# Kernel tuning notes

Hardware: AMD Instinct MI355X
Metric: run time of the kernel (lower is better)

Reference implementation:

```python
import jax, jax.numpy as jnp
import numpy as np

N_NODES = 100000
N_EDGES = 1600000
N_GRAPHS = 128
IN_F, H_F, OUT_F, HID, NCLS = 128, 128, 64, 10, 10

def setup_inputs() -> dict:
    key = jax.random.key(0)
    ks = jax.random.split(key, 12)
    feats = jax.random.normal(ks[0], (N_NODES, IN_F), dtype=jnp.float32)
    src = jax.random.randint(ks[1], (N_EDGES,), 0, N_NODES, dtype=jnp.int32)
    dst = jax.random.randint(ks[2], (N_EDGES,), 0, N_NODES, dtype=jnp.int32)
    graph_ids = jnp.sort(jax.random.randint(ks[3], (N_NODES,), 0, N_GRAPHS, dtype=jnp.int32))
    def glorot(k, shape):
        fan = shape[0] + shape[1]
        return jax.random.normal(k, shape, dtype=jnp.float32) * jnp.sqrt(2.0 / fan)
    return {
        'feats': feats, 'src': src, 'dst': dst, 'graph_ids': graph_ids,
        'W1': glorot(ks[4], (IN_F, H_F)), 'b1': jnp.zeros((H_F,), jnp.float32),
        'W2': glorot(ks[5], (H_F, OUT_F)), 'b2': jnp.zeros((OUT_F,), jnp.float32),
        'fcW1': glorot(ks[6], (OUT_F, HID)), 'fcb1': jnp.zeros((HID,), jnp.float32),
        'fcW2': glorot(ks[7], (HID, NCLS)), 'fcb2': jnp.zeros((NCLS,), jnp.float32),
    }

def _graph_conv(x, W, b, src, dst):
    # DGL GraphConv, norm='both': D_dst^{-1/2} A D_src^{-1/2} X W + b
    ones = jnp.ones((src.shape[0],), x.dtype)
    deg_out = jnp.clip(jax.ops.segment_sum(ones, src, num_segments=N_NODES), 1.0)
    deg_in = jnp.clip(jax.ops.segment_sum(ones, dst, num_segments=N_NODES), 1.0)
    x = x * jax.lax.rsqrt(deg_out)[:, None]
    m = jax.ops.segment_sum(x[src], dst, num_segments=N_NODES)  # gather-scatter over edges
    m = m * jax.lax.rsqrt(deg_in)[:, None]
    return m @ W + b

def reference(feats, src, dst, graph_ids, W1, b1, W2, b2, fcW1, fcb1, fcW2, fcb2):
    h = jax.nn.relu(_graph_conv(feats, W1, b1, src, dst))
    h = jax.nn.relu(_graph_conv(h, W2, b2, src, dst))
    # dgl.mean_nodes: per-graph mean pooling
    sums = jax.ops.segment_sum(h, graph_ids, num_segments=N_GRAPHS)
    counts = jnp.clip(jax.ops.segment_sum(jnp.ones((N_NODES,), h.dtype), graph_ids, num_segments=N_GRAPHS), 1.0)
    pooled = sums / counts[:, None]  # [G, OUT_F]
    z = jax.nn.relu(pooled @ fcW1 + fcb1)
    return jax.nn.softmax(z @ fcW2 + fcb2, axis=1)
```

## Files before the change

kernel.cpp:

```cpp
#include <hip/hip_runtime.h>
#include <hip/hip_bf16.h>

#define N_NODES 100000
#define N_EDGES 1600000
#define N_GRAPHS 128
#define IN_F 128
#define H_F 128
#define OUT_F 64
#define HID 10
#define NCLS 10
#define XPAD 136
#define BSH 7
#define NBUCK 782
#define SBLK 128
#define EPB (N_EDGES / SBLK)
#define NB_PREP 4
#define PCHUNK 8

typedef __attribute__((ext_vector_type(8))) short bf16x8;
typedef __attribute__((ext_vector_type(4))) float f32x4;
typedef __attribute__((ext_vector_type(2))) float f32x2;

__device__ __forceinline__ float bl(unsigned int u) { return __uint_as_float(u << 16); }
__device__ __forceinline__ float bh(unsigned int u) { return __uint_as_float(u & 0xffff0000u); }

__global__ __launch_bounds__(1024) void k_hist2(const int* __restrict__ src, const int* __restrict__ dst,
                                                int* __restrict__ Pd, int* __restrict__ Ps,
                                                const float* __restrict__ W1, const float* __restrict__ W2,
                                                unsigned short* __restrict__ Wt1, unsigned short* __restrict__ Wt2) {
    __shared__ int hd[NBUCK];
    __shared__ int hs[NBUCK];
    const int blk = blockIdx.x;
    if (blk < SBLK) {
        for (int i = threadIdx.x; i < NBUCK; i += 1024) { hd[i] = 0; hs[i] = 0; }
        __syncthreads();
        const int base = blk * EPB;
        for (int i = threadIdx.x; i < EPB; i += 1024) {
            atomicAdd(&hd[dst[base + i] >> BSH], 1);
            atomicAdd(&hs[src[base + i] >> BSH], 1);
        }
        __syncthreads();
        for (int b = threadIdx.x; b < NBUCK; b += 1024) {
            Pd[b * SBLK + blk] = hd[b];
            Ps[b * SBLK + blk] = hs[b];
        }
    } else {
        int t = (blk - SBLK) * 1024 + threadIdx.x;
        const int stride = NB_PREP * 1024;
        for (int i = t; i < 128 * 128; i += stride) {
            int c = i >> 7, k = i & 127;
            __hip_bfloat16 v = __float2bfloat16(W1[k * 128 + c]);
            Wt1[i] = *(unsigned short*)&v;
        }
        for (int i = t; i < 64 * 128; i += stride) {
            int c = i >> 7, k = i & 127;
            __hip_bfloat16 v = __float2bfloat16(W2[k * 64 + c]);
            Wt2[i] = *(unsigned short*)&v;
        }
    }
}

__global__ __launch_bounds__(128) void k_scanA(int* __restrict__ Pd, int* __restrict__ Ps,
                                               int* __restrict__ Td, int* __restrict__ Ts) {
    __shared__ int sc[128];
    const int b = blockIdx.x;
    const int t = threadIdx.x;
    int* P = (b < NBUCK) ? Pd : Ps;
    int* T = (b < NBUCK) ? Td : Ts;
    const int bb = (b < NBUCK) ? b : b - NBUCK;
    int v = P[bb * SBLK + t];
    sc[t] = v;
    __syncthreads();
    for (int off = 1; off < 128; off <<= 1) {
        int u = (t >= off) ? sc[t - off] : 0;
        __syncthreads();
        sc[t] += u;
        __syncthreads();
    }
    P[bb * SBLK + t] = sc[t] - v;
    if (t == 127) T[bb] = sc[127];
}

__global__ __launch_bounds__(1024) void k_scanB(const int* __restrict__ Td, const int* __restrict__ Ts,
                                                int* __restrict__ Bd, int* __restrict__ Bs) {
    __shared__ int sc[1024];
    const int t = threadIdx.x;
    int v = (t < NBUCK) ? Td[t] : 0;
    sc[t] = v;
    __syncthreads();
    for (int off = 1; off < 1024; off <<= 1) {
        int u = (t >= off) ? sc[t - off] : 0;
        __syncthreads();
        sc[t] += u;
        __syncthreads();
    }
    if (t < NBUCK) Bd[t] = sc[t] - v;
    if (t == NBUCK - 1) Bd[NBUCK] = sc[t];
    __syncthreads();
    int v2 = (t < NBUCK) ? Ts[t] : 0;
    sc[t] = v2;
    __syncthreads();
    for (int off = 1; off < 1024; off <<= 1) {
        int u = (t >= off) ? sc[t - off] : 0;
        __syncthreads();
        sc[t] += u;
        __syncthreads();
    }
    if (t < NBUCK) Bs[t] = sc[t] - v2;
    if (t == NBUCK - 1) Bs[NBUCK] = sc[t];
}

__global__ __launch_bounds__(1024) void k_scatter(const int* __restrict__ src, const int* __restrict__ dst,
                                                  const int* __restrict__ Pd, const int* __restrict__ Ps,
                                                  const int* __restrict__ Bd, const int* __restrict__ Bs,
                                                  unsigned int* __restrict__ pb, unsigned char* __restrict__ sb) {
    __shared__ int tk[NBUCK];
    const int b = blockIdx.x;
    const bool isPb = b < SBLK;
    const int blk = isPb ? b : b - SBLK;
    for (int i = threadIdx.x; i < NBUCK; i += 1024) tk[i] = 0;
    __syncthreads();
    const int base = blk * EPB;
    if (isPb) {
        for (int i = threadIdx.x; i < EPB; i += 1024) {
            int d = dst[base + i];
            int s = src[base + i];
            int bd = d >> BSH;
            int t = atomicAdd(&tk[bd], 1);
            pb[Bd[bd] + Pd[bd * SBLK + blk] + t] = ((unsigned)s << 7) | (unsigned)(d & 127);
        }
    } else {
        for (int i = threadIdx.x; i < EPB; i += 1024) {
            int s = src[base + i];
            int bs = s >> BSH;
            int t = atomicAdd(&tk[bs], 1);
            sb[Bs[bs] + Ps[bs * SBLK + blk] + t] = (unsigned char)(s & 127);
        }
    }
}

__global__ __launch_bounds__(256) void k_finalize(const unsigned int* __restrict__ pb, const int* __restrict__ Bd,
                                                  const unsigned char* __restrict__ sb, const int* __restrict__ Bs,
                                                  int* __restrict__ rp, int* __restrict__ cnt_out,
                                                  int* __restrict__ cols) {
    __shared__ int cnt[128];
    __shared__ int exc[128];
    __shared__ int tick[128];
    __shared__ int h[128];
    __shared__ int sc[128];
    const int b = blockIdx.x;
    const int tid = threadIdx.x;
    if (tid < 128) { cnt[tid] = 0; tick[tid] = 0; h[tid] = 0; }
    __syncthreads();
    const int e0 = Bd[b], e1 = Bd[b + 1];
    for (int i = e0 + tid; i < e1; i += 256) atomicAdd(&cnt[pb[i] & 127], 1);
    const int f0 = Bs[b], f1 = Bs[b + 1];
    for (int i = f0 + tid; i < f1; i += 256) atomicAdd(&h[sb[i]], 1);
    __syncthreads();
    if (tid < 128) sc[tid] = cnt[tid];
    __syncthreads();
    for (int off = 1; off < 128; off <<= 1) {
        int u = (tid < 128 && tid >= off) ? sc[tid - off] : 0;
        __syncthreads();
        if (tid < 128) sc[tid] += u;
        __syncthreads();
    }
    if (tid < 128) exc[tid] = sc[tid] - cnt[tid];
    __syncthreads();
    const int node0 = b << BSH;
    if (tid < 128 && node0 + tid < N_NODES) {
        rp[node0 + tid] = e0 + exc[tid];
        cnt_out[node0 + tid] = h[tid];
    }
    if (b == NBUCK - 1 && tid == 0) rp[N_NODES] = N_EDGES;
    for (int i = e0 + tid; i < e1; i += 256) {
        unsigned int p = pb[i];
        int loc = p & 127;
        int t = atomicAdd(&tick[loc], 1);
        cols[e0 + exc[loc] + t] = (int)(p >> 7);
    }
}

__global__ __launch_bounds__(256) void k_gemm1(const float* __restrict__ X,
                                               const unsigned short* __restrict__ Wt,
                                               const int* __restrict__ cnt_out,
                                               unsigned char* __restrict__ Gout) {
    __shared__ __align__(16) unsigned short Xs[32 * XPAD];
    __shared__ __align__(16) unsigned short Ws[128 * XPAD];
    const int tid = threadIdx.x;
    const int row0 = blockIdx.x * 32;

    {
        const float4* X4 = (const float4*)X;
#pragma unroll
        for (int j = 0; j < 4; j++) {
            int i = tid + 256 * j;
            int r = i >> 5, k4 = i & 31;
            float4 x = X4[(size_t)(row0 + r) * 32 + k4];
            __hip_bfloat162 lo = __float22bfloat162_rn({x.x, x.y});
            __hip_bfloat162 hi = __float22bfloat162_rn({x.z, x.w});
            uint2 u;
            u.x = *(unsigned int*)&lo;
            u.y = *(unsigned int*)&hi;
            *(uint2*)&Xs[r * XPAD + k4 * 4] = u;
        }
    }
    {
        const uint2* W2 = (const uint2*)Wt;
#pragma unroll
        for (int j = 0; j < 16; j++) {
            int i = tid + 256 * j;
            int cc = i >> 5, kk = i & 31;
            uint2 u = W2[(size_t)cc * 32 + kk];
            *(uint2*)&Ws[cc * XPAD + kk * 4] = u;
        }
    }
    __syncthreads();

    const int lane = tid & 63;
    const int wv = tid >> 6;
    const int m = lane & 15;
    const int q = lane >> 4;
    const int cg = wv * 32;

    f32x4 acc00 = {0.f, 0.f, 0.f, 0.f}, acc01 = {0.f, 0.f, 0.f, 0.f};
    f32x4 acc10 = {0.f, 0.f, 0.f, 0.f}, acc11 = {0.f, 0.f, 0.f, 0.f};
#pragma unroll
    for (int ks = 0; ks < 4; ks++) {
        int kb = ks * 32 + q * 8;
        bf16x8 a0 = *(const bf16x8*)&Xs[m * XPAD + kb];
        bf16x8 a1 = *(const bf16x8*)&Xs[(16 + m) * XPAD + kb];
        bf16x8 b0 = *(const bf16x8*)&Ws[(cg + m) * XPAD + kb];
        bf16x8 b1 = *(const bf16x8*)&Ws[(cg + 16 + m) * XPAD + kb];
        acc00 = __builtin_amdgcn_mfma_f32_16x16x32_bf16(a0, b0, acc00, 0, 0, 0);
        acc01 = __builtin_amdgcn_mfma_f32_16x16x32_bf16(a0, b1, acc01, 0, 0, 0);
        acc10 = __builtin_amdgcn_mfma_f32_16x16x32_bf16(a1, b0, acc10, 0, 0, 0);
        acc11 = __builtin_amdgcn_mfma_f32_16x16x32_bf16(a1, b1, acc11, 0, 0, 0);
    }
#pragma unroll
    for (int r = 0; r < 4; r++) {
        int rowA = row0 + q * 4 + r;
        int rowB = rowA + 16;
        float sA = rsqrtf((float)max(cnt_out[rowA], 1));
        float sB = rsqrtf((float)max(cnt_out[rowB], 1));
        unsigned int pkA = __builtin_amdgcn_cvt_pk_fp8_f32(acc00[r] * sA, acc01[r] * sA, 0, false);
        unsigned int pkB = __builtin_amdgcn_cvt_pk_fp8_f32(acc10[r] * sB, acc11[r] * sB, 0, false);
        unsigned char* gA = Gout + (size_t)rowA * 128 + cg + m;
        gA[0]  = (unsigned char)(pkA & 0xffu);
        gA[16] = (unsigned char)((pkA >> 8) & 0xffu);
        unsigned char* gB = Gout + (size_t)rowB * 128 + cg + m;
        gB[0]  = (unsigned char)(pkB & 0xffu);
        gB[16] = (unsigned char)((pkB >> 8) & 0xffu);
    }
}

template <int TOTF, bool XBF16, bool OUT_FP8>
__global__ __launch_bounds__(256) void k_gemm_mfma(const void* __restrict__ Xv,
                                                   const unsigned short* __restrict__ Wt,
                                                   const int* __restrict__ cnt_out,
                                                   void* __restrict__ GoutV) {
    __shared__ __align__(16) unsigned short Xs[32 * XPAD];
    __shared__ __align__(16) unsigned short Ws[64 * XPAD];
    const int tid = threadIdx.x;
    const int cbase = blockIdx.y * 64;
    const int row0 = blockIdx.x * 32;

    if constexpr (XBF16) {
        const uint2* X2 = (const uint2*)Xv;
#pragma unroll
        for (int j = 0; j < 4; j++) {
            int i = tid + 256 * j;
            int r = i >> 5, kk = i & 31;
            uint2 u = X2[(size_t)(row0 + r) * 32 + kk];
            *(uint2*)&Xs[r * XPAD + kk * 4] = u;
        }
    } else {
        const float4* X4 = (const float4*)Xv;
#pragma unroll
        for (int j = 0; j < 4; j++) {
            int i = tid + 256 * j;
            int r = i >> 5, k4 = i & 31;
            float4 x = X4[(size_t)(row0 + r) * 32 + k4];
            __hip_bfloat162 lo = __float22bfloat162_rn({x.x, x.y});
            __hip_bfloat162 hi = __float22bfloat162_rn({x.z, x.w});
            uint2 u;
            u.x = *(unsigned int*)&lo;
            u.y = *(unsigned int*)&hi;
            *(uint2*)&Xs[r * XPAD + k4 * 4] = u;
        }
    }
    {
        const uint2* W2 = (const uint2*)Wt;
#pragma unroll
        for (int j = 0; j < 8; j++) {
            int i = tid + 256 * j;
            int c = i >> 5, kk = i & 31;
            uint2 u = W2[(size_t)(cbase + c) * 32 + kk];
            *(uint2*)&Ws[c * XPAD + kk * 4] = u;
        }
    }
    __syncthreads();

    const int lane = tid & 63;
    const int wv = tid >> 6;
    const int m = lane & 15;
    const int q = lane >> 4;
    const int roff = (wv & 1) * 16;
    const int coff = (wv >> 1) * 32;

    f32x4 acc0 = {0.f, 0.f, 0.f, 0.f}, acc1 = {0.f, 0.f, 0.f, 0.f};
#pragma unroll
    for (int ks = 0; ks < 4; ks++) {
        int kb = ks * 32 + q * 8;
        bf16x8 a  = *(const bf16x8*)&Xs[(roff + m) * XPAD + kb];
        bf16x8 b0 = *(const bf16x8*)&Ws[(coff + m) * XPAD + kb];
        bf16x8 b1 = *(const bf16x8*)&Ws[(coff + 16 + m) * XPAD + kb];
        acc0 = __builtin_amdgcn_mfma_f32_16x16x32_bf16(a, b0, acc0, 0, 0, 0);
        acc1 = __builtin_amdgcn_mfma_f32_16x16x32_bf16(a, b1, acc1, 0, 0, 0);
    }
#pragma unroll
    for (int r = 0; r < 4; r++) {
        int row = row0 + roff + q * 4 + r;
        float s = rsqrtf((float)max(cnt_out[row], 1));
        int col0 = cbase + coff + m;
        if constexpr (OUT_FP8) {
            unsigned int pk = __builtin_amdgcn_cvt_pk_fp8_f32(acc0[r] * s, acc1[r] * s, 0, false);
            unsigned char* gp = (unsigned char*)GoutV + (size_t)row * TOTF + col0;
            gp[0]  = (unsigned char)(pk & 0xffu);
            gp[16] = (unsigned char)((pk >> 8) & 0xffu);
        } else {
            unsigned short* Gout = (unsigned short*)GoutV;
            __hip_bfloat16 o0 = __float2bfloat16(acc0[r] * s);
            __hip_bfloat16 o1 = __float2bfloat16(acc1[r] * s);
            Gout[(size_t)row * TOTF + col0]      = *(unsigned short*)&o0;
            Gout[(size_t)row * TOTF + col0 + 16] = *(unsigned short*)&o1;
        }
    }
}

__global__ __launch_bounds__(256) void k_spmm128f8(const unsigned short* __restrict__ G,
                                                   const int* __restrict__ rp,
                                                   const int* __restrict__ cols,
                                                   const float* __restrict__ bias,
                                                   unsigned int* __restrict__ H) {
    const int lane = threadIdx.x & 63;
    const int wave = threadIdx.x >> 6;
    const int v = blockIdx.x * 4 + wave;
    const int b0 = __builtin_amdgcn_readfirstlane(rp[v]);
    const int e0 = __builtin_amdgcn_readfirstlane(rp[v + 1]);
    const int deg = e0 - b0;
    const unsigned short* gl = G + lane;
    f32x2 acc = {0.f, 0.f};
    int j = 0;
    while (j + 16 <= deg) {
        unsigned int u[16];
#pragma unroll
        for (int k = 0; k < 16; k++) {
            int s = cols[b0 + j + k];
            u[k] = gl[(size_t)s * 64];
        }
#pragma unroll
        for (int k = 0; k < 16; k++) acc += __builtin_amdgcn_cvt_pk_f32_fp8(u[k], false);
        j += 16;
    }
    if (j + 8 <= deg) {
        unsigned int u[8];
#pragma unroll
        for (int k = 0; k < 8; k++) { int s = cols[b0 + j + k]; u[k] = gl[(size_t)s * 64]; }
#pragma unroll
        for (int k = 0; k < 8; k++) acc += __builtin_amdgcn_cvt_pk_f32_fp8(u[k], false);
        j += 8;
    }
    if (j + 4 <= deg) {
        unsigned int u[4];
#pragma unroll
        for (int k = 0; k < 4; k++) { int s = cols[b0 + j + k]; u[k] = gl[(size_t)s * 64]; }
#pragma unroll
        for (int k = 0; k < 4; k++) acc += __builtin_amdgcn_cvt_pk_f32_fp8(u[k], false);
        j += 4;
    }
    if (j + 2 <= deg) {
        unsigned int u0, u1;
        { int s = cols[b0 + j];     u0 = gl[(size_t)s * 64]; }
        { int s = cols[b0 + j + 1]; u1 = gl[(size_t)s * 64]; }
        acc += __builtin_amdgcn_cvt_pk_f32_fp8(u0, false);
        acc += __builtin_amdgcn_cvt_pk_f32_fp8(u1, false);
        j += 2;
    }
    if (j < deg) {
        int s = cols[b0 + j];
        unsigned int u = gl[(size_t)s * 64];
        acc += __builtin_amdgcn_cvt_pk_f32_fp8(u, false);
    }
    const float rs = rsqrtf((float)max(deg, 1));
    const float2 bb = *(const float2*)&bias[2 * lane];
    __hip_bfloat162 p = __float22bfloat162_rn({fmaxf(fmaf(acc.x, rs, bb.x), 0.f),
                                               fmaxf(fmaf(acc.y, rs, bb.y), 0.f)});
    H[(size_t)v * 64 + lane] = *(unsigned int*)&p;
}

__global__ __launch_bounds__(256) void k_spmm64f8(const unsigned char* __restrict__ G,
                                                  const int* __restrict__ rp,
                                                  const int* __restrict__ cols,
                                                  const float* __restrict__ bias,
                                                  unsigned short* __restrict__ H) {
    const int lane = threadIdx.x & 63;
    const int wave = threadIdx.x >> 6;
    const int v = blockIdx.x * 4 + wave;
    const int b0 = __builtin_amdgcn_readfirstlane(rp[v]);
    const int e0 = __builtin_amdgcn_readfirstlane(rp[v + 1]);
    const int deg = e0 - b0;
    const unsigned char* gl = G + lane;
    f32x2 acc = {0.f, 0.f};
    int j = 0;
    while (j + 16 <= deg) {
        unsigned int u[16];
#pragma unroll
        for (int k = 0; k < 16; k++) {
            int s = cols[b0 + j + k];
            u[k] = gl[(size_t)s * 64];
        }
#pragma unroll
        for (int k = 0; k < 16; k++) acc += __builtin_amdgcn_cvt_pk_f32_fp8(u[k], false);
        j += 16;
    }
    if (j + 8 <= deg) {
        unsigned int u[8];
#pragma unroll
        for (int k = 0; k < 8; k++) { int s = cols[b0 + j + k]; u[k] = gl[(size_t)s * 64]; }
#pragma unroll
        for (int k = 0; k < 8; k++) acc += __builtin_amdgcn_cvt_pk_f32_fp8(u[k], false);
        j += 8;
    }
    if (j + 4 <= deg) {
        unsigned int u[4];
#pragma unroll
        for (int k = 0; k < 4; k++) { int s = cols[b0 + j + k]; u[k] = gl[(size_t)s * 64]; }
#pragma unroll
        for (int k = 0; k < 4; k++) acc += __builtin_amdgcn_cvt_pk_f32_fp8(u[k], false);
        j += 4;
    }
    if (j + 2 <= deg) {
        unsigned int u0, u1;
        { int s = cols[b0 + j];     u0 = gl[(size_t)s * 64]; }
        { int s = cols[b0 + j + 1]; u1 = gl[(size_t)s * 64]; }
        acc += __builtin_amdgcn_cvt_pk_f32_fp8(u0, false);
        acc += __builtin_amdgcn_cvt_pk_f32_fp8(u1, false);
        j += 2;
    }
    if (j < deg) {
        int s = cols[b0 + j];
        unsigned int u = gl[(size_t)s * 64];
        acc += __builtin_amdgcn_cvt_pk_f32_fp8(u, false);
    }
    const float rs = rsqrtf((float)max(deg, 1));
    const float b = bias[lane];
    __hip_bfloat16 o = __float2bfloat16(fmaxf(fmaf(acc.x, rs, b), 0.f));
    H[(size_t)v * 64 + lane] = *(unsigned short*)&o;
}

__global__ __launch_bounds__(256) void k_pool(const unsigned short* __restrict__ h2,
                                              const int* __restrict__ gid,
                                              float* __restrict__ part) {
    __shared__ int se[2];
    __shared__ float red[16][16][4];
    const int cpart = blockIdx.x;
    const int g = blockIdx.y;
    const int tid = threadIdx.x;
    if (tid < 2) {
        int target = g + tid;
        int lo = 0, hi = N_NODES;
        while (lo < hi) {
            int mid = (lo + hi) >> 1;
            if (gid[mid] < target) lo = mid + 1; else hi = mid;
        }
        se[tid] = lo;
    }
    __syncthreads();
    const int s = se[0], e = se[1];
    const int chunk = (e - s + PCHUNK - 1) / PCHUNK;
    const int lo = s + cpart * chunk;
    const int hi = min(lo + chunk, e);
    const int r = tid >> 4, cp = tid & 15;
    float a0 = 0.f, a1 = 0.f, a2 = 0.f, a3 = 0.f;
    const uint2* H = (const uint2*)h2;
    for (int v = lo + r; v < hi; v += 16) {
        uint2 u = H[(size_t)v * 16 + cp];
        a0 += bl(u.x); a1 += bh(u.x); a2 += bl(u.y); a3 += bh(u.y);
    }
    red[r][cp][0] = a0; red[r][cp][1] = a1; red[r][cp][2] = a2; red[r][cp][3] = a3;
    for (int off = 8; off > 0; off >>= 1) {
        __syncthreads();
        if (r < off) {
#pragma unroll
            for (int k = 0; k < 4; k++) red[r][cp][k] += red[r + off][cp][k];
        }
    }
    __syncthreads();
    if (r == 0) {
        float4 o = {red[0][cp][0], red[0][cp][1], red[0][cp][2], red[0][cp][3]};
        *(float4*)&part[((size_t)cpart * N_GRAPHS + g) * 64 + 4 * cp] = o;
    }
}

__global__ __launch_bounds__(64) void k_mlp(const float* __restrict__ part,
                                            const int* __restrict__ gid,
                                            const float* __restrict__ fcW1,
                                            const float* __restrict__ fcb1,
                                            const float* __restrict__ fcW2,
                                            const float* __restrict__ fcb2,
                                            float* __restrict__ out) {
    __shared__ int se[2];
    __shared__ float p[64];
    __shared__ float z[10];
    __shared__ float l[10];
    __shared__ float red[2];
    const int g = blockIdx.x;
    const int t = threadIdx.x;
    if (t < 2) {
        int target = g + t;
        int lo = 0, hi = N_NODES;
        while (lo < hi) {
            int mid = (lo + hi) >> 1;
            if (gid[mid] < target) lo = mid + 1; else hi = mid;
        }
        se[t] = lo;
    }
    __syncthreads();
    const int cnt = max(se[1] - se[0], 1);
    float a = 0.f;
#pragma unroll
    for (int c = 0; c < PCHUNK; c++) a += part[((size_t)c * N_GRAPHS + g) * 64 + t];
    p[t] = a / (float)cnt;
    __syncthreads();
    if (t < 10) {
        float acc = fcb1[t];
        for (int k = 0; k < 64; k++) acc = fmaf(p[k], fcW1[k * 10 + t], acc);
        z[t] = fmaxf(acc, 0.f);
    }
    __syncthreads();
    if (t < 10) {
        float acc = fcb2[t];
        for (int k = 0; k < 10; k++) acc = fmaf(z[k], fcW2[k * 10 + t], acc);
        l[t] = acc;
    }
    __syncthreads();
    if (t == 0) {
        float m = l[0];
        for (int i = 1; i < 10; i++) m = fmaxf(m, l[i]);
        float ssum = 0.f;
        for (int i = 0; i < 10; i++) ssum += expf(l[i] - m);
        red[0] = m;
        red[1] = ssum;
    }
    __syncthreads();
    if (t < 10) out[g * 10 + t] = expf(l[t] - red[0]) / red[1];
}

extern "C" void kernel_launch(void* const* d_in, const int* in_sizes, int n_in,
                              void* d_out, int out_size, void* d_ws, size_t ws_size,
                              hipStream_t stream) {
    const float* feats = (const float*)d_in[0];
    const int* src = (const int*)d_in[1];
    const int* dst = (const int*)d_in[2];
    const int* gid = (const int*)d_in[3];
    const float* W1 = (const float*)d_in[4];
    const float* b1 = (const float*)d_in[5];
    const float* W2 = (const float*)d_in[6];
    const float* b2 = (const float*)d_in[7];
    const float* fcW1 = (const float*)d_in[8];
    const float* fcb1 = (const float*)d_in[9];
    const float* fcW2 = (const float*)d_in[10];
    const float* fcb2 = (const float*)d_in[11];
    float* out = (float*)d_out;

    char* w = (char*)d_ws;
    size_t off = 0;
    auto alloc = [&](size_t bytes) -> void* {
        void* p = w + off;
        off = (off + bytes + 255) & ~(size_t)255;
        return p;
    };
    int* cnt_out = (int*)alloc(N_NODES * 4);
    int* rp      = (int*)alloc((N_NODES + 1) * 4);
    int* cols    = (int*)alloc((size_t)N_EDGES * 4);
    int* Pd      = (int*)alloc(NBUCK * SBLK * 4);
    int* Ps      = (int*)alloc(NBUCK * SBLK * 4);
    int* Td      = (int*)alloc(NBUCK * 4);
    int* Ts      = (int*)alloc(NBUCK * 4);
    int* Bd      = (int*)alloc((NBUCK + 1) * 4);
    int* Bs      = (int*)alloc((NBUCK + 1) * 4);
    unsigned int* pb  = (unsigned int*)alloc((size_t)N_EDGES * 4);
    unsigned char* sb = (unsigned char*)alloc((size_t)N_EDGES);
    unsigned short* Wt1 = (unsigned short*)alloc(128 * 128 * 2);
    unsigned short* Wt2 = (unsigned short*)alloc(64 * 128 * 2);
    unsigned char* g1 = (unsigned char*)alloc((size_t)N_NODES * 128);
    unsigned short* h1 = (unsigned short*)alloc((size_t)N_NODES * 128 * 2);
    unsigned char* g2 = (unsigned char*)alloc((size_t)N_NODES * 64);
    unsigned short* h2 = (unsigned short*)alloc((size_t)N_NODES * 64 * 2);
    float* part = (float*)alloc((size_t)PCHUNK * N_GRAPHS * 64 * 4);

    k_hist2<<<SBLK + NB_PREP, 1024, 0, stream>>>(src, dst, Pd, Ps, W1, W2, Wt1, Wt2);
    k_scanA<<<2 * NBUCK, 128, 0, stream>>>(Pd, Ps, Td, Ts);
    k_scanB<<<1, 1024, 0, stream>>>(Td, Ts, Bd, Bs);
    k_scatter<<<2 * SBLK, 1024, 0, stream>>>(src, dst, Pd, Ps, Bd, Bs, pb, sb);
    k_finalize<<<NBUCK, 256, 0, stream>>>(pb, Bd, sb, Bs, rp, cnt_out, cols);

    k_gemm1<<<N_NODES / 32, 256, 0, stream>>>(feats, Wt1, cnt_out, g1);
    k_spmm128f8<<<N_NODES / 4, 256, 0, stream>>>((const unsigned short*)g1, rp, cols, b1, (unsigned int*)h1);

    k_gemm_mfma<64, true, true><<<dim3(N_NODES / 32, 1), 256, 0, stream>>>(h1, Wt2, cnt_out, g2);
    k_spmm64f8<<<N_NODES / 4, 256, 0, stream>>>(g2, rp, cols, b2, (unsigned short*)h2);

    k_pool<<<dim3(PCHUNK, N_GRAPHS), 256, 0, stream>>>(h2, gid, part);
    k_mlp<<<N_GRAPHS, 64, 0, stream>>>(part, gid, fcW1, fcb1, fcW2, fcb2, out);
}
```

Baseline: 279.7 us.

## Compute out-degree with global atomics and process two nodes per wave in SpMM

Out-degree counting moves from a bucketed sort pass (src histogram, scan, byte scatter, per-bucket count) to direct global atomic increments into a zeroed count array, which removes half of the CSR-build work. Both SpMM kernels now have each wave handle two consecutive destination nodes, interleaving their gathers in blocks of eight, to raise memory-level parallelism and halve the block count. The trade-offs are global atomic contention on 100k counters and a larger per-wave register footprint, plus extra tail code.

```diff
diff --git a/kernel.cpp b/kernel.cpp
--- a/kernel.cpp
+++ b/kernel.cpp
@@ -24,26 +24,28 @@
 __device__ __forceinline__ float bl(unsigned int u) { return __uint_as_float(u << 16); }
 __device__ __forceinline__ float bh(unsigned int u) { return __uint_as_float(u & 0xffff0000u); }
 
+__global__ __launch_bounds__(256) void k_zero(int* __restrict__ p, int n) {
+    int i = blockIdx.x * 256 + threadIdx.x;
+    int stride = gridDim.x * 256;
+    for (; i < n; i += stride) p[i] = 0;
+}
+
 __global__ __launch_bounds__(1024) void k_hist2(const int* __restrict__ src, const int* __restrict__ dst,
-                                                int* __restrict__ Pd, int* __restrict__ Ps,
+                                                int* __restrict__ Pd, int* __restrict__ cnt_out,
                                                 const float* __restrict__ W1, const float* __restrict__ W2,
                                                 unsigned short* __restrict__ Wt1, unsigned short* __restrict__ Wt2) {
     __shared__ int hd[NBUCK];
-    __shared__ int hs[NBUCK];
     const int blk = blockIdx.x;
     if (blk < SBLK) {
-        for (int i = threadIdx.x; i < NBUCK; i += 1024) { hd[i] = 0; hs[i] = 0; }
+        for (int i = threadIdx.x; i < NBUCK; i += 1024) hd[i] = 0;
         __syncthreads();
         const int base = blk * EPB;
         for (int i = threadIdx.x; i < EPB; i += 1024) {
             atomicAdd(&hd[dst[base + i] >> BSH], 1);
-            atomicAdd(&hs[src[base + i] >> BSH], 1);
-        }
-        __syncthreads();
-        for (int b = threadIdx.x; b < NBUCK; b += 1024) {
-            Pd[b * SBLK + blk] = hd[b];
-            Ps[b * SBLK + blk] = hs[b];
-        }
+            atomicAdd(&cnt_out[src[base + i]], 1);
+        }
+        __syncthreads();
+        for (int b = threadIdx.x; b < NBUCK; b += 1024) Pd[b * SBLK + blk] = hd[b];
     } else {
         int t = (blk - SBLK) * 1024 + threadIdx.x;
         const int stride = NB_PREP * 1024;
@@ -60,15 +62,11 @@
     }
 }
 
-__global__ __launch_bounds__(128) void k_scanA(int* __restrict__ Pd, int* __restrict__ Ps,
-                                               int* __restrict__ Td, int* __restrict__ Ts) {
+__global__ __launch_bounds__(128) void k_scanA(int* __restrict__ Pd, int* __restrict__ Td) {
     __shared__ int sc[128];
     const int b = blockIdx.x;
     const int t = threadIdx.x;
-    int* P = (b < NBUCK) ? Pd : Ps;
-    int* T = (b < NBUCK) ? Td : Ts;
-    const int bb = (b < NBUCK) ? b : b - NBUCK;
-    int v = P[bb * SBLK + t];
+    int v = Pd[b * SBLK + t];
     sc[t] = v;
     __syncthreads();
     for (int off = 1; off < 128; off <<= 1) {
@@ -77,12 +75,11 @@
         sc[t] += u;
         __syncthreads();
     }
-    P[bb * SBLK + t] = sc[t] - v;
-    if (t == 127) T[bb] = sc[127];
-}
-
-__global__ __launch_bounds__(1024) void k_scanB(const int* __restrict__ Td, const int* __restrict__ Ts,
-                                                int* __restrict__ Bd, int* __restrict__ Bs) {
+    Pd[b * SBLK + t] = sc[t] - v;
+    if (t == 127) Td[b] = sc[127];
+}
+
+__global__ __launch_bounds__(1024) void k_scanB(const int* __restrict__ Td, int* __restrict__ Bd) {
     __shared__ int sc[1024];
     const int t = threadIdx.x;
     int v = (t < NBUCK) ? Td[t] : 0;
@@ -96,66 +93,37 @@
     }
     if (t < NBUCK) Bd[t] = sc[t] - v;
     if (t == NBUCK - 1) Bd[NBUCK] = sc[t];
-    __syncthreads();
-    int v2 = (t < NBUCK) ? Ts[t] : 0;
-    sc[t] = v2;
-    __syncthreads();
-    for (int off = 1; off < 1024; off <<= 1) {
-        int u = (t >= off) ? sc[t - off] : 0;
-        __syncthreads();
-        sc[t] += u;
-        __syncthreads();
-    }
-    if (t < NBUCK) Bs[t] = sc[t] - v2;
-    if (t == NBUCK - 1) Bs[NBUCK] = sc[t];
 }
 
 __global__ __launch_bounds__(1024) void k_scatter(const int* __restrict__ src, const int* __restrict__ dst,
-                                                  const int* __restrict__ Pd, const int* __restrict__ Ps,
-                                                  const int* __restrict__ Bd, const int* __restrict__ Bs,
-                                                  unsigned int* __restrict__ pb, unsigned char* __restrict__ sb) {
+                                                  const int* __restrict__ Pd, const int* __restrict__ Bd,
+                                                  unsigned int* __restrict__ pb) {
     __shared__ int tk[NBUCK];
-    const int b = blockIdx.x;
-    const bool isPb = b < SBLK;
-    const int blk = isPb ? b : b - SBLK;
+    const int blk = blockIdx.x;
     for (int i = threadIdx.x; i < NBUCK; i += 1024) tk[i] = 0;
     __syncthreads();
     const int base = blk * EPB;
-    if (isPb) {
-        for (int i = threadIdx.x; i < EPB; i += 1024) {
-            int d = dst[base + i];
-            int s = src[base + i];
-            int bd = d >> BSH;
-            int t = atomicAdd(&tk[bd], 1);
-            pb[Bd[bd] + Pd[bd * SBLK + blk] + t] = ((unsigned)s << 7) | (unsigned)(d & 127);
-        }
-    } else {
-        for (int i = threadIdx.x; i < EPB; i += 1024) {
-            int s = src[base + i];
-            int bs = s >> BSH;
-            int t = atomicAdd(&tk[bs], 1);
-            sb[Bs[bs] + Ps[bs * SBLK + blk] + t] = (unsigned char)(s & 127);
-        }
+    for (int i = threadIdx.x; i < EPB; i += 1024) {
+        int d = dst[base + i];
+        int s = src[base + i];
+        int bd = d >> BSH;
+        int t = atomicAdd(&tk[bd], 1);
+        pb[Bd[bd] + Pd[bd * SBLK + blk] + t] = ((unsigned)s << 7) | (unsigned)(d & 127);
     }
 }
 
 __global__ __launch_bounds__(256) void k_finalize(const unsigned int* __restrict__ pb, const int* __restrict__ Bd,
-                                                  const unsigned char* __restrict__ sb, const int* __restrict__ Bs,
-                                                  int* __restrict__ rp, int* __restrict__ cnt_out,
-                                                  int* __restrict__ cols) {
+                                                  int* __restrict__ rp, int* __restrict__ cols) {
     __shared__ int cnt[128];
     __shared__ int exc[128];
     __shared__ int tick[128];
-    __shared__ int h[128];
     __shared__ int sc[128];
     const int b = blockIdx.x;
     const int tid = threadIdx.x;
-    if (tid < 128) { cnt[tid] = 0; tick[tid] = 0; h[tid] = 0; }
+    if (tid < 128) { cnt[tid] = 0; tick[tid] = 0; }
     __syncthreads();
     const int e0 = Bd[b], e1 = Bd[b + 1];
     for (int i = e0 + tid; i < e1; i += 256) atomicAdd(&cnt[pb[i] & 127], 1);
-    const int f0 = Bs[b], f1 = Bs[b + 1];
-    for (int i = f0 + tid; i < f1; i += 256) atomicAdd(&h[sb[i]], 1);
     __syncthreads();
     if (tid < 128) sc[tid] = cnt[tid];
     __syncthreads();
@@ -168,10 +136,7 @@
     if (tid < 128) exc[tid] = sc[tid] - cnt[tid];
     __syncthreads();
     const int node0 = b << BSH;
-    if (tid < 128 && node0 + tid < N_NODES) {
-        rp[node0 + tid] = e0 + exc[tid];
-        cnt_out[node0 + tid] = h[tid];
-    }
+    if (tid < 128 && node0 + tid < N_NODES) rp[node0 + tid] = e0 + exc[tid];
     if (b == NBUCK - 1 && tid == 0) rp[N_NODES] = N_EDGES;
     for (int i = e0 + tid; i < e1; i += 256) {
         unsigned int p = pb[i];
@@ -338,6 +303,88 @@
     }
 }
 
+__device__ __forceinline__ void tail128(const unsigned short* __restrict__ gl, const int* __restrict__ cols,
+                                        int b, int d, int j, f32x2& acc) {
+    while (j + 16 <= d) {
+        unsigned int u[16];
+#pragma unroll
+        for (int k = 0; k < 16; k++) { int s = cols[b + j + k]; u[k] = gl[(size_t)s * 64]; }
+#pragma unroll
+        for (int k = 0; k < 16; k++) acc += __builtin_amdgcn_cvt_pk_f32_fp8(u[k], false);
+        j += 16;
+    }
+    if (j + 8 <= d) {
+        unsigned int u[8];
+#pragma unroll
+        for (int k = 0; k < 8; k++) { int s = cols[b + j + k]; u[k] = gl[(size_t)s * 64]; }
+#pragma unroll
+        for (int k = 0; k < 8; k++) acc += __builtin_amdgcn_cvt_pk_f32_fp8(u[k], false);
+        j += 8;
+    }
+    if (j + 4 <= d) {
+        unsigned int u[4];
+#pragma unroll
+        for (int k = 0; k < 4; k++) { int s = cols[b + j + k]; u[k] = gl[(size_t)s * 64]; }
+#pragma unroll
+        for (int k = 0; k < 4; k++) acc += __builtin_amdgcn_cvt_pk_f32_fp8(u[k], false);
+        j += 4;
+    }
+    if (j + 2 <= d) {
+        unsigned int u0, u1;
+        { int s = cols[b + j];     u0 = gl[(size_t)s * 64]; }
+        { int s = cols[b + j + 1]; u1 = gl[(size_t)s * 64]; }
+        acc += __builtin_amdgcn_cvt_pk_f32_fp8(u0, false);
+        acc += __builtin_amdgcn_cvt_pk_f32_fp8(u1, false);
+        j += 2;
+    }
+    if (j < d) {
+        int s = cols[b + j];
+        unsigned int u = gl[(size_t)s * 64];
+        acc += __builtin_amdgcn_cvt_pk_f32_fp8(u, false);
+    }
+}
+
+__device__ __forceinline__ void tail64(const unsigned char* __restrict__ gl, const int* __restrict__ cols,
+                                       int b, int d, int j, f32x2& acc) {
+    while (j + 16 <= d) {
+        unsigned int u[16];
+#pragma unroll
+        for (int k = 0; k < 16; k++) { int s = cols[b + j + k]; u[k] = gl[(size_t)s * 64]; }
+#pragma unroll
+        for (int k = 0; k < 16; k++) acc += __builtin_amdgcn_cvt_pk_f32_fp8(u[k], false);
+        j += 16;
+    }
+    if (j + 8 <= d) {
+        unsigned int u[8];
+#pragma unroll
+        for (int k = 0; k < 8; k++) { int s = cols[b + j + k]; u[k] = gl[(size_t)s * 64]; }
+#pragma unroll
+        for (int k = 0; k < 8; k++) acc += __builtin_amdgcn_cvt_pk_f32_fp8(u[k], false);
+        j += 8;
+    }
+    if (j + 4 <= d) {
+        unsigned int u[4];
+#pragma unroll
+        for (int k = 0; k < 4; k++) { int s = cols[b + j + k]; u[k] = gl[(size_t)s * 64]; }
+#pragma unroll
+        for (int k = 0; k < 4; k++) acc += __builtin_amdgcn_cvt_pk_f32_fp8(u[k], false);
+        j += 4;
+    }
+    if (j + 2 <= d) {
+        unsigned int u0, u1;
+        { int s = cols[b + j];     u0 = gl[(size_t)s * 64]; }
+        { int s = cols[b + j + 1]; u1 = gl[(size_t)s * 64]; }
+        acc += __builtin_amdgcn_cvt_pk_f32_fp8(u0, false);
+        acc += __builtin_amdgcn_cvt_pk_f32_fp8(u1, false);
+        j += 2;
+    }
+    if (j < d) {
+        int s = cols[b + j];
+        unsigned int u = gl[(size_t)s * 64];
+        acc += __builtin_amdgcn_cvt_pk_f32_fp8(u, false);
+    }
+}
+
 __global__ __launch_bounds__(256) void k_spmm128f8(const unsigned short* __restrict__ G,
                                                    const int* __restrict__ rp,
                                                    const int* __restrict__ cols,
@@ -345,58 +392,43 @@
                                                    unsigned int* __restrict__ H) {
     const int lane = threadIdx.x & 63;
     const int wave = threadIdx.x >> 6;
-    const int v = blockIdx.x * 4 + wave;
-    const int b0 = __builtin_amdgcn_readfirstlane(rp[v]);
-    const int e0 = __builtin_amdgcn_readfirstlane(rp[v + 1]);
-    const int deg = e0 - b0;
+    const int v0 = (blockIdx.x * 4 + wave) * 2;
+    const int b0 = __builtin_amdgcn_readfirstlane(rp[v0]);
+    const int b1 = __builtin_amdgcn_readfirstlane(rp[v0 + 1]);
+    const int e1 = __builtin_amdgcn_readfirstlane(rp[v0 + 2]);
+    const int dA = b1 - b0, dB = e1 - b1;
     const unsigned short* gl = G + lane;
-    f32x2 acc = {0.f, 0.f};
-    int j = 0;
-    while (j + 16 <= deg) {
-        unsigned int u[16];
-#pragma unroll
-        for (int k = 0; k < 16; k++) {
-            int s = cols[b0 + j + k];
-            u[k] = gl[(size_t)s * 64];
-        }
-#pragma unroll
-        for (int k = 0; k < 16; k++) acc += __builtin_amdgcn_cvt_pk_f32_fp8(u[k], false);
-        j += 16;
-    }
-    if (j + 8 <= deg) {
-        unsigned int u[8];
-#pragma unroll
-        for (int k = 0; k < 8; k++) { int s = cols[b0 + j + k]; u[k] = gl[(size_t)s * 64]; }
-#pragma unroll
-        for (int k = 0; k < 8; k++) acc += __builtin_amdgcn_cvt_pk_f32_fp8(u[k], false);
-        j += 8;
-    }
-    if (j + 4 <= deg) {
-        unsigned int u[4];
-#pragma unroll
-        for (int k = 0; k < 4; k++) { int s = cols[b0 + j + k]; u[k] = gl[(size_t)s * 64]; }
-#pragma unroll
-        for (int k = 0; k < 4; k++) acc += __builtin_amdgcn_cvt_pk_f32_fp8(u[k], false);
-        j += 4;
-    }
-    if (j + 2 <= deg) {
-        unsigned int u0, u1;
-        { int s = cols[b0 + j];     u0 = gl[(size_t)s * 64]; }
-        { int s = cols[b0 + j + 1]; u1 = gl[(size_t)s * 64]; }
-        acc += __builtin_amdgcn_cvt_pk_f32_fp8(u0, false);
-        acc += __builtin_amdgcn_cvt_pk_f32_fp8(u1, false);
-        j += 2;
-    }
-    if (j < deg) {
-        int s = cols[b0 + j];
-        unsigned int u = gl[(size_t)s * 64];
-        acc += __builtin_amdgcn_cvt_pk_f32_fp8(u, false);
-    }
-    const float rs = rsqrtf((float)max(deg, 1));
-    const float2 bb = *(const float2*)&bias[2 * lane];
-    __hip_bfloat162 p = __float22bfloat162_rn({fmaxf(fmaf(acc.x, rs, bb.x), 0.f),
-                                               fmaxf(fmaf(acc.y, rs, bb.y), 0.f)});
-    H[(size_t)v * 64 + lane] = *(unsigned int*)&p;
+    f32x2 aA = {0.f, 0.f}, aB = {0.f, 0.f};
+    int ja = 0, jb = 0;
+    while (ja + 8 <= dA && jb + 8 <= dB) {
+        unsigned int u[8], w[8];
+#pragma unroll
+        for (int k = 0; k < 8; k++) { int s = cols[b0 + ja + k]; u[k] = gl[(size_t)s * 64]; }
+#pragma unroll
+        for (int k = 0; k < 8; k++) { int s = cols[b1 + jb + k]; w[k] = gl[(size_t)s * 64]; }
+#pragma unroll
+        for (int k = 0; k < 8; k++) aA += __builtin_amdgcn_cvt_pk_f32_fp8(u[k], false);
+#pragma unroll
+        for (int k = 0; k < 8; k++) aB += __builtin_amdgcn_cvt_pk_f32_fp8(w[k], false);
+        ja += 8; jb += 8;
+    }
+    tail128(gl, cols, b0, dA, ja, aA);
+    tail128(gl, cols, b1, dB, jb, aB);
+
+    {
+        const float rs = rsqrtf((float)max(dA, 1));
+        const float2 bb = *(const float2*)&bias[2 * lane];
+        __hip_bfloat162 p = __float22bfloat162_rn({fmaxf(fmaf(aA.x, rs, bb.x), 0.f),
+                                                   fmaxf(fmaf(aA.y, rs, bb.y), 0.f)});
+        H[(size_t)v0 * 64 + lane] = *(unsigned int*)&p;
+    }
+    {
+        const float rs = rsqrtf((float)max(dB, 1));
+        const float2 bb = *(const float2*)&bias[2 * lane];
+        __hip_bfloat162 p = __float22bfloat162_rn({fmaxf(fmaf(aB.x, rs, bb.x), 0.f),
+                                                   fmaxf(fmaf(aB.y, rs, bb.y), 0.f)});
+        H[(size_t)(v0 + 1) * 64 + lane] = *(unsigned int*)&p;
+    }
 }
 
 __global__ __launch_bounds__(256) void k_spmm64f8(const unsigned char* __restrict__ G,
@@ -406,57 +438,39 @@
                                                   unsigned short* __restrict__ H) {
     const int lane = threadIdx.x & 63;
     const int wave = threadIdx.x >> 6;
-    const int v = blockIdx.x * 4 + wave;
-    const int b0 = __builtin_amdgcn_readfirstlane(rp[v]);
-    const int e0 = __builtin_amdgcn_readfirstlane(rp[v + 1]);
-    const int deg = e0 - b0;
+    const int v0 = (blockIdx.x * 4 + wave) * 2;
+    const int b0 = __builtin_amdgcn_readfirstlane(rp[v0]);
+    const int b1 = __builtin_amdgcn_readfirstlane(rp[v0 + 1]);
+    const int e1 = __builtin_amdgcn_readfirstlane(rp[v0 + 2]);
+    const int dA = b1 - b0, dB = e1 - b1;
     const unsigned char* gl = G + lane;
-    f32x2 acc = {0.f, 0.f};
-    int j = 0;
-    while (j + 16 <= deg) {
-        unsigned int u[16];
-#pragma unroll
-        for (int k = 0; k < 16; k++) {
-            int s = cols[b0 + j + k];
-            u[k] = gl[(size_t)s * 64];
-        }
-#pragma unroll
-        for (int k = 0; k < 16; k++) acc += __builtin_amdgcn_cvt_pk_f32_fp8(u[k], false);
-        j += 16;
-    }
-    if (j + 8 <= deg) {
-        unsigned int u[8];
-#pragma unroll
-        for (int k = 0; k < 8; k++) { int s = cols[b0 + j + k]; u[k] = gl[(size_t)s * 64]; }
-#pragma unroll
-        for (int k = 0; k < 8; k++) acc += __builtin_amdgcn_cvt_pk_f32_fp8(u[k], false);
-        j += 8;
-    }
-    if (j + 4 <= deg) {
-        unsigned int u[4];
-#pragma unroll
-        for (int k = 0; k < 4; k++) { int s = cols[b0 + j + k]; u[k] = gl[(size_t)s * 64]; }
-#pragma unroll
-        for (int k = 0; k < 4; k++) acc += __builtin_amdgcn_cvt_pk_f32_fp8(u[k], false);
-        j += 4;
-    }
-    if (j + 2 <= deg) {
-        unsigned int u0, u1;
-        { int s = cols[b0 + j];     u0 = gl[(size_t)s * 64]; }
-        { int s = cols[b0 + j + 1]; u1 = gl[(size_t)s * 64]; }
-        acc += __builtin_amdgcn_cvt_pk_f32_fp8(u0, false);
-        acc += __builtin_amdgcn_cvt_pk_f32_fp8(u1, false);
-        j += 2;
-    }
-    if (j < deg) {
-        int s = cols[b0 + j];
-        unsigned int u = gl[(size_t)s * 64];
-        acc += __builtin_amdgcn_cvt_pk_f32_fp8(u, false);
-    }
-    const float rs = rsqrtf((float)max(deg, 1));
-    const float b = bias[lane];
-    __hip_bfloat16 o = __float2bfloat16(fmaxf(fmaf(acc.x, rs, b), 0.f));
-    H[(size_t)v * 64 + lane] = *(unsigned short*)&o;
+    f32x2 aA = {0.f, 0.f}, aB = {0.f, 0.f};
+    int ja = 0, jb = 0;
+    while (ja + 8 <= dA && jb + 8 <= dB) {
+        unsigned int u[8], w[8];
+#pragma unroll
+        for (int k = 0; k < 8; k++) { int s = cols[b0 + ja + k]; u[k] = gl[(size_t)s * 64]; }
+#pragma unroll
+        for (int k = 0; k < 8; k++) { int s = cols[b1 + jb + k]; w[k] = gl[(size_t)s * 64]; }
+#pragma unroll
+        for (int k = 0; k < 8; k++) aA += __builtin_amdgcn_cvt_pk_f32_fp8(u[k], false);
+#pragma unroll
+        for (int k = 0; k < 8; k++) aB += __builtin_amdgcn_cvt_pk_f32_fp8(w[k], false);
+        ja += 8; jb += 8;
+    }
+    tail64(gl, cols, b0, dA, ja, aA);
+    tail64(gl, cols, b1, dB, jb, aB);
+
+    {
+        const float rs = rsqrtf((float)max(dA, 1));
+        __hip_bfloat16 o = __float2bfloat16(fmaxf(fmaf(aA.x, rs, bias[lane]), 0.f));
+        H[(size_t)v0 * 64 + lane] = *(unsigned short*)&o;
+    }
+    {
+        const float rs = rsqrtf((float)max(dB, 1));
+        __hip_bfloat16 o = __float2bfloat16(fmaxf(fmaf(aB.x, rs, bias[lane]), 0.f));
+        H[(size_t)(v0 + 1) * 64 + lane] = *(unsigned short*)&o;
+    }
 }
 
 __global__ __launch_bounds__(256) void k_pool(const unsigned short* __restrict__ h2,
@@ -585,13 +599,9 @@
     int* rp      = (int*)alloc((N_NODES + 1) * 4);
     int* cols    = (int*)alloc((size_t)N_EDGES * 4);
     int* Pd      = (int*)alloc(NBUCK * SBLK * 4);
-    int* Ps      = (int*)alloc(NBUCK * SBLK * 4);
     int* Td      = (int*)alloc(NBUCK * 4);
-    int* Ts      = (int*)alloc(NBUCK * 4);
     int* Bd      = (int*)alloc((NBUCK + 1) * 4);
-    int* Bs      = (int*)alloc((NBUCK + 1) * 4);
     unsigned int* pb  = (unsigned int*)alloc((size_t)N_EDGES * 4);
-    unsigned char* sb = (unsigned char*)alloc((size_t)N_EDGES);
     unsigned short* Wt1 = (unsigned short*)alloc(128 * 128 * 2);
     unsigned short* Wt2 = (unsigned short*)alloc(64 * 128 * 2);
     unsigned char* g1 = (unsigned char*)alloc((size_t)N_NODES * 128);
@@ -600,17 +610,18 @@
     unsigned short* h2 = (unsigned short*)alloc((size_t)N_NODES * 64 * 2);
     float* part = (float*)alloc((size_t)PCHUNK * N_GRAPHS * 64 * 4);
 
-    k_hist2<<<SBLK + NB_PREP, 1024, 0, stream>>>(src, dst, Pd, Ps, W1, W2, Wt1, Wt2);
-    k_scanA<<<2 * NBUCK, 128, 0, stream>>>(Pd, Ps, Td, Ts);
-    k_scanB<<<1, 1024, 0, stream>>>(Td, Ts, Bd, Bs);
-    k_scatter<<<2 * SBLK, 1024, 0, stream>>>(src, dst, Pd, Ps, Bd, Bs, pb, sb);
-    k_finalize<<<NBUCK, 256, 0, stream>>>(pb, Bd, sb, Bs, rp, cnt_out, cols);
+    k_zero<<<256, 256, 0, stream>>>(cnt_out, N_NODES);
+    k_hist2<<<SBLK + NB_PREP, 1024, 0, stream>>>(src, dst, Pd, cnt_out, W1, W2, Wt1, Wt2);
+    k_scanA<<<NBUCK, 128, 0, stream>>>(Pd, Td);
+    k_scanB<<<1, 1024, 0, stream>>>(Td, Bd);
+    k_scatter<<<SBLK, 1024, 0, stream>>>(src, dst, Pd, Bd, pb);
+    k_finalize<<<NBUCK, 256, 0, stream>>>(pb, Bd, rp, cols);
 
     k_gemm1<<<N_NODES / 32, 256, 0, stream>>>(feats, Wt1, cnt_out, g1);
-    k_spmm128f8<<<N_NODES / 4, 256, 0, stream>>>((const unsigned short*)g1, rp, cols, b1, (unsigned int*)h1);
+    k_spmm128f8<<<N_NODES / 8, 256, 0, stream>>>((const unsigned short*)g1, rp, cols, b1, (unsigned int*)h1);
 
     k_gemm_mfma<64, true, true><<<dim3(N_NODES / 32, 1), 256, 0, stream>>>(h1, Wt2, cnt_out, g2);
-    k_spmm64f8<<<N_NODES / 4, 256, 0, stream>>>(g2, rp, cols, b2, (unsigned short*)h2);
+    k_spmm64f8<<<N_NODES / 8, 256, 0, stream>>>(g2, rp, cols, b2, (unsigned short*)h2);
 
     k_pool<<<dim3(PCHUNK, N_GRAPHS), 256, 0, stream>>>(h2, gid, part);
     k_mlp<<<N_GRAPHS, 64, 0, stream>>>(part, gid, fcW1, fcb1, fcW2, fcb2, out);
```

New measurement: 320.5 us. 1.15x slower.
